# Kernel tuning notes

Measured on AMD Instinct MI355X. Metric: run time of the kernel, lower is better.

Reference implementation:

```python
import jax, jax.numpy as jnp
import numpy as np

B = 128
INPUT_SIZE = 1024
VALUE_CAP = 32768      # value_capacity (memory_size of value SDM)
VALUE_SPARSITY = 32
ASSOC_CAP = 4096       # associative_capacity; projected_size = ASSOC_CAP * 1
ASSOC_SPARSITY = 32
PROJ_DIM = ASSOC_CAP   # associative_projection_scale_factor = 1


def _row_normalize(x):
    return x / jnp.linalg.norm(x, axis=1, keepdims=True)


def setup_inputs() -> dict:
    key = jax.random.key(0)
    k1, k2, k3, k4, k5 = jax.random.split(key, 5)
    keys = jax.random.normal(k1, (B, INPUT_SIZE), dtype=jnp.float32)
    # value_memory.proj: row-normalized random projection [VALUE_CAP, INPUT_SIZE]
    value_proj = _row_normalize(jax.random.normal(k2, (VALUE_CAP, INPUT_SIZE), dtype=jnp.float32))
    # clique_encoder: randn / sqrt(projected_size) [VALUE_CAP, PROJ_DIM]
    clique_encoder = jax.random.normal(k3, (VALUE_CAP, PROJ_DIM), dtype=jnp.float32) / np.sqrt(PROJ_DIM)
    # associative_memory.proj: row-normalized [ASSOC_CAP, PROJ_DIM]
    assoc_proj = _row_normalize(jax.random.normal(k4, (ASSOC_CAP, PROJ_DIM), dtype=jnp.float32))
    # associative_memory.mem_value [ASSOC_CAP, VALUE_CAP] (zeros in a fresh
    # module; randomized here so retrieval output is non-trivial)
    assoc_mem_value = jax.random.normal(k5, (ASSOC_CAP, VALUE_CAP), dtype=jnp.float32) * 0.01
    return {
        "keys": keys,
        "value_proj": value_proj,
        "clique_encoder": clique_encoder,
        "assoc_proj": assoc_proj,
        "assoc_mem_value": assoc_mem_value,
    }


def reference(keys, value_proj, clique_encoder, assoc_proj, assoc_mem_value):
    # AssociativeSparseDistributedMemory.get_cliques(keys)
    # 1) value_memory.encode: dense matmul + topk addressing
    scores = keys @ value_proj.T                          # [B, VALUE_CAP]
    _, clique_idx = jax.lax.top_k(scores, VALUE_SPARSITY)  # [B, K]
    # 2) _dense_projection: gather K rows of clique_encoder, sum, scale, l2-normalize
    p = clique_encoder[clique_idx].sum(axis=1)            # [B, PROJ_DIM]
    p = p / np.sqrt(VALUE_SPARSITY)
    norm = jnp.linalg.norm(p, axis=-1, keepdims=True)
    p = p / jnp.maximum(norm, 1e-12)                      # F.normalize semantics
    # 3) associative_memory.get_value: encode + gather-sum retrieval
    scores2 = p @ assoc_proj.T                            # [B, ASSOC_CAP]
    _, assoc_idx = jax.lax.top_k(scores2, ASSOC_SPARSITY)  # [B, K2]
    cliques = assoc_mem_value[assoc_idx].sum(axis=1)      # [B, VALUE_CAP]
    return cliques
```

## Files before the change

kernel.cpp:

```cpp
#include <hip/hip_runtime.h>
#include <math.h>

#define TOPK 32
#define NVAL 32768
#define D 4096

typedef __attribute__((ext_vector_type(8))) short bf16x8;
typedef __attribute__((ext_vector_type(4))) float f32x4;

__device__ inline short f2bf(float x) {
    union { float f; unsigned u; } v; v.f = x;
    unsigned r = v.u + 0x7fffu + ((v.u >> 16) & 1u);
    return (short)(r >> 16);
}

__global__ __launch_bounds__(256) void cvt_bf16_kernel(
    const float* __restrict__ in, short* __restrict__ out, int n4)
{
    int i = blockIdx.x * 256 + threadIdx.x;
    if (i < n4) {
        float4 v = ((const float4*)in)[i];
        short4 o = {f2bf(v.x), f2bf(v.y), f2bf(v.z), f2bf(v.w)};
        ((short4*)out)[i] = o;
    }
}

__global__ __launch_bounds__(256) void gemm_bf16_kernel(
    const short* __restrict__ Abf, const float* __restrict__ B,
    float* __restrict__ C, int K, int N, int klen)
{
    const int t = threadIdx.x;
    const int lane = t & 63;
    const int w = t >> 6;
    const int ntile = blockIdx.x * 64 + w * 16;
    const int k0 = blockIdx.y * klen;
    float* Cb = C + (size_t)blockIdx.y * 128 * N;

    const int kfrag = (lane >> 4) * 8;
    const float* bp = B + (size_t)(ntile + (lane & 15)) * K + kfrag;
    const short* ap = Abf + (size_t)(lane & 15) * K + kfrag;

    f32x4 acc[8];
    #pragma unroll
    for (int j = 0; j < 8; ++j) acc[j] = (f32x4){0.f, 0.f, 0.f, 0.f};

    float4 x0 = *(const float4*)(bp + k0);
    float4 x1 = *(const float4*)(bp + k0 + 4);
    float4 y0 = *(const float4*)(bp + k0 + 32);
    float4 y1 = *(const float4*)(bp + k0 + 36);
    for (int ks = k0; ks < k0 + klen; ks += 32) {
        bf16x8 af;
        af[0] = f2bf(x0.x); af[1] = f2bf(x0.y); af[2] = f2bf(x0.z); af[3] = f2bf(x0.w);
        af[4] = f2bf(x1.x); af[5] = f2bf(x1.y); af[6] = f2bf(x1.z); af[7] = f2bf(x1.w);
        x0 = y0; x1 = y1;
        if (ks + 64 < k0 + klen) {
            y0 = *(const float4*)(bp + ks + 64);
            y1 = *(const float4*)(bp + ks + 68);
        }
        #pragma unroll
        for (int j = 0; j < 8; ++j) {
            bf16x8 kf = *(const bf16x8*)(ap + (size_t)16 * K * j + ks);
            acc[j] = __builtin_amdgcn_mfma_f32_16x16x32_bf16(af, kf, acc[j], 0, 0, 0);
        }
    }
    const int crow0 = ntile + (lane >> 4) * 4;
    const int ccol = lane & 15;
    #pragma unroll
    for (int j = 0; j < 8; ++j) {
        float4 o = {acc[j][0], acc[j][1], acc[j][2], acc[j][3]};
        *(float4*)(Cb + (size_t)(16 * j + ccol) * N + crow0) = o;
    }
}

__global__ __launch_bounds__(256) void reduceS_kernel(
    const float* __restrict__ part, float* __restrict__ out, int elems4, int S)
{
    int i = blockIdx.x * blockDim.x + threadIdx.x;
    if (i < elems4) {
        float4 s = {0.f, 0.f, 0.f, 0.f};
        for (int r = 0; r < S; ++r) {
            float4 v = *(const float4*)(part + (size_t)r * elems4 * 4 + (size_t)i * 4);
            s.x += v.x; s.y += v.y; s.z += v.z; s.w += v.w;
        }
        *(float4*)(out + (size_t)i * 4) = s;
    }
}

#define FNT 512
__global__ __launch_bounds__(FNT) void filter64_kernel(
    const float* __restrict__ scores, int n, int* __restrict__ cand_out)
{
    __shared__ unsigned long long lkey[8 * FNT];
    __shared__ unsigned long long wkey[FNT / 64];
    const int t = threadIdx.x;
    const float* row = scores + (size_t)blockIdx.x * n;

    unsigned long long kl[8];
    #pragma unroll
    for (int i = 0; i < 8; ++i) kl[i] = 0ull;

    const int nvec = n >> 2;
    for (int base = t; base < nvec; base += FNT) {
        float4 x4 = *(const float4*)(row + base * 4);
        float xs[4] = {x4.x, x4.y, x4.z, x4.w};
        #pragma unroll
        for (int q = 0; q < 4; ++q) {
            unsigned fb = __float_as_uint(xs[q]);
            unsigned s = (fb & 0x80000000u) ? ~fb : (fb | 0x80000000u);
            unsigned idx = (unsigned)(base * 4 + q);
            unsigned long long key = ((unsigned long long)s << 32) | (unsigned long long)(~idx);
            if (key > kl[7]) {
                unsigned long long c = key;
                #pragma unroll
                for (int i = 0; i < 8; ++i) {
                    unsigned long long old = kl[i];
                    bool gt = c > old;
                    kl[i] = gt ? c : old;
                    c = gt ? old : c;
                }
            }
        }
    }
    #pragma unroll
    for (int i = 0; i < 8; ++i) lkey[i * FNT + t] = kl[i];
    __syncthreads();

    int h = 0;
    int* out = cand_out + blockIdx.x * 64;
    for (int sel = 0; sel < 64; ++sel) {
        unsigned long long cnd = (h < 8) ? lkey[h * FNT + t] : 0ull;
        unsigned long long b = cnd;
        #pragma unroll
        for (int s2 = 1; s2 < 64; s2 <<= 1) {
            unsigned long long o = __shfl_xor(b, s2);
            if (o > b) b = o;
        }
        if ((t & 63) == 0) wkey[t >> 6] = b;
        __syncthreads();
        unsigned long long g = wkey[0];
        #pragma unroll
        for (int ww = 1; ww < FNT / 64; ++ww) {
            unsigned long long o = wkey[ww];
            if (o > g) g = o;
        }
        if (t == 0) out[sel] = (int)(~(unsigned)g);
        if (cnd == g) h++;
        __syncthreads();
    }
}

__global__ __launch_bounds__(256) void rescore_part_kernel(
    const float* __restrict__ Arows, const float* __restrict__ Brows,
    const int* __restrict__ cand, int K, unsigned long long* __restrict__ keybuf)
{
    __shared__ float arow[4096];
    const int t = threadIdx.x;
    const int b = blockIdx.x;
    const int s = blockIdx.y;
    for (int i = t; i < (K >> 2); i += 256)
        ((float4*)arow)[i] = ((const float4*)(Arows + (size_t)b * K))[i];
    __syncthreads();
    const int w = t >> 6, lane = t & 63;
    for (int c = s * 32 + w; c < s * 32 + 32; c += 4) {
        int r = cand[b * 64 + c];
        const float4* bp = (const float4*)(Brows + (size_t)r * K);
        float sum = 0.f;
        for (int q = lane; q < (K >> 2); q += 64) {
            float4 bv = bp[q];
            float4 av = ((float4*)arow)[q];
            sum = fmaf(av.x, bv.x, fmaf(av.y, bv.y, fmaf(av.z, bv.z, fmaf(av.w, bv.w, sum))));
        }
        #pragma unroll
        for (int sh = 1; sh < 64; sh <<= 1) sum += __shfl_xor(sum, sh);
        if (lane == 0) {
            unsigned fb = __float_as_uint(sum);
            unsigned ss = (fb & 0x80000000u) ? ~fb : (fb | 0x80000000u);
            keybuf[b * 64 + c] = ((unsigned long long)ss << 32) | (unsigned long long)(~(unsigned)r);
        }
    }
}

__global__ __launch_bounds__(64) void top32_keys_kernel(
    const unsigned long long* __restrict__ keybuf, int* __restrict__ idx_out)
{
    const int b = blockIdx.x, t = threadIdx.x;
    unsigned long long key = keybuf[b * 64 + t];
    int* out = idx_out + b * TOPK;
    for (int sel = 0; sel < TOPK; ++sel) {
        unsigned long long g = key;
        #pragma unroll
        for (int sh = 1; sh < 64; sh <<= 1) {
            unsigned long long o = __shfl_xor(g, sh);
            if (o > g) g = o;
        }
        if (t == 0) out[sel] = (int)(~(unsigned)g);
        if (key == g) key = 0ull;
    }
}

__global__ __launch_bounds__(256) void gather_sum_kernel(
    const float* __restrict__ enc, const int* __restrict__ idx,
    float* __restrict__ p_raw, float* __restrict__ ssp)
{
    __shared__ int rows[TOPK];
    __shared__ float red[256];
    const int t = threadIdx.x;
    const int half = blockIdx.x;
    const int b = blockIdx.y;
    if (t < TOPK) rows[t] = idx[b * TOPK + t];
    __syncthreads();
    const int base = half * 2048 + t * 8;
    float4 a0 = {}, a1 = {};
    #pragma unroll 4
    for (int r = 0; r < TOPK; ++r) {
        const float* src = enc + (size_t)rows[r] * D + base;
        float4 v0 = *(const float4*)(src);
        float4 v1 = *(const float4*)(src + 4);
        a0.x += v0.x; a0.y += v0.y; a0.z += v0.z; a0.w += v0.w;
        a1.x += v1.x; a1.y += v1.y; a1.z += v1.z; a1.w += v1.w;
    }
    const float sc = 0.17677669529663687f;
    a0.x *= sc; a0.y *= sc; a0.z *= sc; a0.w *= sc;
    a1.x *= sc; a1.y *= sc; a1.z *= sc; a1.w *= sc;
    float ss = a0.x*a0.x + a0.y*a0.y + a0.z*a0.z + a0.w*a0.w
             + a1.x*a1.x + a1.y*a1.y + a1.z*a1.z + a1.w*a1.w;
    red[t] = ss;
    __syncthreads();
    for (int s = 128; s > 0; s >>= 1) {
        if (t < s) red[t] += red[t + s];
        __syncthreads();
    }
    if (t == 0) ssp[b * 2 + half] = red[0];
    float* dst = p_raw + (size_t)b * D + base;
    *(float4*)dst = a0;
    *(float4*)(dst + 4) = a1;
}

__global__ __launch_bounds__(256) void normalize_kernel(
    const float* __restrict__ p_raw, const float* __restrict__ ssp,
    float* __restrict__ p, short* __restrict__ p_bf)
{
    const int b = blockIdx.x, t = threadIdx.x;
    const float rinv = 1.0f / fmaxf(sqrtf(ssp[b * 2] + ssp[b * 2 + 1]), 1e-12f);
    for (int i = t; i < (D >> 2); i += 256) {
        float4 v = ((const float4*)(p_raw + (size_t)b * D))[i];
        float4 o = {v.x * rinv, v.y * rinv, v.z * rinv, v.w * rinv};
        ((float4*)(p + (size_t)b * D))[i] = o;
        short4 ob = {f2bf(o.x), f2bf(o.y), f2bf(o.z), f2bf(o.w)};
        ((short4*)(p_bf + (size_t)b * D))[i] = ob;
    }
}

__global__ __launch_bounds__(256) void gather_out_kernel(
    const float* __restrict__ mem, const int* __restrict__ idx, float* __restrict__ out)
{
    extern __shared__ float throttle[];
    __shared__ int rows[TOPK];
    const int t = threadIdx.x;
    const int b = blockIdx.x;
    const int chunk = blockIdx.y;
    if (t < TOPK) rows[t] = idx[b * TOPK + t];
    __syncthreads();
    const int off = chunk * 2048 + t * 8;
    float4 a0 = {}, a1 = {};
    #pragma unroll 4
    for (int r = 0; r < TOPK; ++r) {
        const float* src = mem + (size_t)rows[r] * NVAL + off;
        float4 v0 = *(const float4*)(src);
        float4 v1 = *(const float4*)(src + 4);
        a0.x += v0.x; a0.y += v0.y; a0.z += v0.z; a0.w += v0.w;
        a1.x += v1.x; a1.y += v1.y; a1.z += v1.z; a1.w += v1.w;
    }
    if (rows[0] < 0) { throttle[t] = a0.x; out[0] = throttle[t + 1]; }
    float* dst = out + (size_t)b * NVAL + off;
    *(float4*)dst = a0;
    *(float4*)(dst + 4) = a1;
}

extern "C" void kernel_launch(void* const* d_in, const int* in_sizes, int n_in,
                              void* d_out, int out_size, void* d_ws, size_t ws_size,
                              hipStream_t stream) {
    const float* keys            = (const float*)d_in[0];
    const float* value_proj      = (const float*)d_in[1];
    const float* clique_encoder  = (const float*)d_in[2];
    const float* assoc_proj      = (const float*)d_in[3];
    const float* assoc_mem_value = (const float*)d_in[4];
    float* out = (float*)d_out;

    char* ws = (char*)d_ws;
    short* keysbf = (short*)(ws);
    float* s1a    = (float*)(ws + 262144);
    float* p_raw  = (float*)(ws + 17039360);
    float* p      = (float*)(ws + 19136512);
    short* p_bf   = (short*)(ws + 21233664);
    float* part2  = (float*)(ws + 22282240);
    float* s2a    = (float*)(ws + 30670848);
    int*   cand1  = (int*)  (ws + 32768000);
    int*   cand2  = (int*)  (ws + 32800768);
    int*   idx1   = (int*)  (ws + 32833536);
    int*   idx2   = (int*)  (ws + 32849920);
    unsigned long long* keyb1 = (unsigned long long*)(ws + 32866304);
    unsigned long long* keyb2 = (unsigned long long*)(ws + 32931840);
    float* ssp    = (float*)(ws + 32997376);

    cvt_bf16_kernel<<<128, 256, 0, stream>>>(keys, keysbf, 32768);
    gemm_bf16_kernel<<<dim3(512, 1), 256, 0, stream>>>(keysbf, value_proj, s1a, 1024, NVAL, 1024);
    filter64_kernel<<<128, FNT, 0, stream>>>(s1a, NVAL, cand1);
    rescore_part_kernel<<<dim3(128, 2), 256, 0, stream>>>(keys, value_proj, cand1, 1024, keyb1);
    top32_keys_kernel<<<128, 64, 0, stream>>>(keyb1, idx1);
    gather_sum_kernel<<<dim3(2, 128), 256, 0, stream>>>(clique_encoder, idx1, p_raw, ssp);
    normalize_kernel<<<128, 256, 0, stream>>>(p_raw, ssp, p, p_bf);
    gemm_bf16_kernel<<<dim3(64, 4), 256, 0, stream>>>(p_bf, assoc_proj, part2, 4096, D, 1024);
    reduceS_kernel<<<512, 256, 0, stream>>>(part2, s2a, 131072, 4);
    filter64_kernel<<<128, FNT, 0, stream>>>(s2a, D, cand2);
    rescore_part_kernel<<<dim3(128, 2), 256, 0, stream>>>(p, assoc_proj, cand2, 4096, keyb2);
    top32_keys_kernel<<<128, 64, 0, stream>>>(keyb2, idx2);
    gather_out_kernel<<<dim3(128, 16), 256, 40960, stream>>>(assoc_mem_value, idx2, out);
}
```

Before: 445.2 us.

## Use split-bf16 GEMM for second stage and skip rescore when top-32 gap is clear

The second scoring GEMM now uses a hi/lo bf16 split of the normalized projection (three MFMAs per tile) so its scores are near-fp32 accurate. A new select2 kernel fuses the split-K reduction into the top-64 filter, writes the top-32 indices directly, and flags rows whose 32nd/33rd gap is below a threshold. Only flagged rows run the exact fp32 rescore and top-32 pass. The first GEMM gains a deeper prefetch and the first rescore grid doubles in the y dimension. The price is three times the MFMA work plus an extra lo buffer, and correctness now depends on the 1e-5 gap threshold being safe.

```diff
diff --git a/kernel.cpp b/kernel.cpp
--- a/kernel.cpp
+++ b/kernel.cpp
@@ -12,6 +12,10 @@
     union { float f; unsigned u; } v; v.f = x;
     unsigned r = v.u + 0x7fffu + ((v.u >> 16) & 1u);
     return (short)(r >> 16);
+}
+__device__ inline float bf2f(short h) {
+    union { unsigned u; float f; } v; v.u = ((unsigned)(unsigned short)h) << 16;
+    return v.f;
 }
 
 __global__ __launch_bounds__(256) void cvt_bf16_kernel(
@@ -27,7 +31,54 @@
 
 __global__ __launch_bounds__(256) void gemm_bf16_kernel(
     const short* __restrict__ Abf, const float* __restrict__ B,
-    float* __restrict__ C, int K, int N, int klen)
+    float* __restrict__ C, int K, int N)
+{
+    const int t = threadIdx.x;
+    const int lane = t & 63;
+    const int w = t >> 6;
+    const int ntile = blockIdx.x * 64 + w * 16;
+
+    const int kfrag = (lane >> 4) * 8;
+    const float* bp = B + (size_t)(ntile + (lane & 15)) * K + kfrag;
+    const short* ap = Abf + (size_t)(lane & 15) * K + kfrag;
+
+    f32x4 acc[8];
+    #pragma unroll
+    for (int j = 0; j < 8; ++j) acc[j] = (f32x4){0.f, 0.f, 0.f, 0.f};
+
+    float4 x0 = *(const float4*)(bp);
+    float4 x1 = *(const float4*)(bp + 4);
+    float4 y0 = *(const float4*)(bp + 32);
+    float4 y1 = *(const float4*)(bp + 36);
+    float4 z0 = *(const float4*)(bp + 64);
+    float4 z1 = *(const float4*)(bp + 68);
+    for (int ks = 0; ks < K; ks += 32) {
+        bf16x8 af;
+        af[0] = f2bf(x0.x); af[1] = f2bf(x0.y); af[2] = f2bf(x0.z); af[3] = f2bf(x0.w);
+        af[4] = f2bf(x1.x); af[5] = f2bf(x1.y); af[6] = f2bf(x1.z); af[7] = f2bf(x1.w);
+        x0 = y0; x1 = y1; y0 = z0; y1 = z1;
+        if (ks + 96 < K) {
+            z0 = *(const float4*)(bp + ks + 96);
+            z1 = *(const float4*)(bp + ks + 100);
+        }
+        #pragma unroll
+        for (int j = 0; j < 8; ++j) {
+            bf16x8 kf = *(const bf16x8*)(ap + (size_t)16 * K * j + ks);
+            acc[j] = __builtin_amdgcn_mfma_f32_16x16x32_bf16(af, kf, acc[j], 0, 0, 0);
+        }
+    }
+    const int crow0 = ntile + (lane >> 4) * 4;
+    const int ccol = lane & 15;
+    #pragma unroll
+    for (int j = 0; j < 8; ++j) {
+        float4 o = {acc[j][0], acc[j][1], acc[j][2], acc[j][3]};
+        *(float4*)(C + (size_t)(16 * j + ccol) * N + crow0) = o;
+    }
+}
+
+__global__ __launch_bounds__(256) void gemm_split_kernel(
+    const short* __restrict__ Ahi, const short* __restrict__ Alo,
+    const float* __restrict__ B, float* __restrict__ C, int K, int N, int klen)
 {
     const int t = threadIdx.x;
     const int lane = t & 63;
@@ -38,7 +89,8 @@
 
     const int kfrag = (lane >> 4) * 8;
     const float* bp = B + (size_t)(ntile + (lane & 15)) * K + kfrag;
-    const short* ap = Abf + (size_t)(lane & 15) * K + kfrag;
+    const short* aph = Ahi + (size_t)(lane & 15) * K + kfrag;
+    const short* apl = Alo + (size_t)(lane & 15) * K + kfrag;
 
     f32x4 acc[8];
     #pragma unroll
@@ -49,18 +101,26 @@
     float4 y0 = *(const float4*)(bp + k0 + 32);
     float4 y1 = *(const float4*)(bp + k0 + 36);
     for (int ks = k0; ks < k0 + klen; ks += 32) {
-        bf16x8 af;
-        af[0] = f2bf(x0.x); af[1] = f2bf(x0.y); af[2] = f2bf(x0.z); af[3] = f2bf(x0.w);
-        af[4] = f2bf(x1.x); af[5] = f2bf(x1.y); af[6] = f2bf(x1.z); af[7] = f2bf(x1.w);
+        float xs[8] = {x0.x, x0.y, x0.z, x0.w, x1.x, x1.y, x1.z, x1.w};
         x0 = y0; x1 = y1;
         if (ks + 64 < k0 + klen) {
             y0 = *(const float4*)(bp + ks + 64);
             y1 = *(const float4*)(bp + ks + 68);
         }
+        bf16x8 bh, bl;
+        #pragma unroll
+        for (int q = 0; q < 8; ++q) {
+            short h = f2bf(xs[q]);
+            bh[q] = h;
+            bl[q] = f2bf(xs[q] - bf2f(h));
+        }
         #pragma unroll
         for (int j = 0; j < 8; ++j) {
-            bf16x8 kf = *(const bf16x8*)(ap + (size_t)16 * K * j + ks);
-            acc[j] = __builtin_amdgcn_mfma_f32_16x16x32_bf16(af, kf, acc[j], 0, 0, 0);
+            bf16x8 kh = *(const bf16x8*)(aph + (size_t)16 * K * j + ks);
+            bf16x8 kl = *(const bf16x8*)(apl + (size_t)16 * K * j + ks);
+            acc[j] = __builtin_amdgcn_mfma_f32_16x16x32_bf16(bh, kh, acc[j], 0, 0, 0);
+            acc[j] = __builtin_amdgcn_mfma_f32_16x16x32_bf16(bl, kh, acc[j], 0, 0, 0);
+            acc[j] = __builtin_amdgcn_mfma_f32_16x16x32_bf16(bh, kl, acc[j], 0, 0, 0);
         }
     }
     const int crow0 = ntile + (lane >> 4) * 4;
@@ -69,20 +129,6 @@
     for (int j = 0; j < 8; ++j) {
         float4 o = {acc[j][0], acc[j][1], acc[j][2], acc[j][3]};
         *(float4*)(Cb + (size_t)(16 * j + ccol) * N + crow0) = o;
-    }
-}
-
-__global__ __launch_bounds__(256) void reduceS_kernel(
-    const float* __restrict__ part, float* __restrict__ out, int elems4, int S)
-{
-    int i = blockIdx.x * blockDim.x + threadIdx.x;
-    if (i < elems4) {
-        float4 s = {0.f, 0.f, 0.f, 0.f};
-        for (int r = 0; r < S; ++r) {
-            float4 v = *(const float4*)(part + (size_t)r * elems4 * 4 + (size_t)i * 4);
-            s.x += v.x; s.y += v.y; s.z += v.z; s.w += v.w;
-        }
-        *(float4*)(out + (size_t)i * 4) = s;
     }
 }
 
@@ -149,19 +195,98 @@
     }
 }
 
+__global__ __launch_bounds__(FNT) void select2_kernel(
+    const float* __restrict__ part, int n, int* __restrict__ idx_out,
+    int* __restrict__ cand_out, int* __restrict__ flags)
+{
+    __shared__ unsigned long long lkey[8 * FNT];
+    __shared__ unsigned long long wkey[FNT / 64];
+    const int t = threadIdx.x;
+    const int b = blockIdx.x;
+
+    unsigned long long kl[8];
+    #pragma unroll
+    for (int i = 0; i < 8; ++i) kl[i] = 0ull;
+
+    const int nvec = n >> 2;
+    for (int base = t; base < nvec; base += FNT) {
+        float4 s0 = *(const float4*)(part + ((size_t)0 * 128 + b) * n + base * 4);
+        float4 s1 = *(const float4*)(part + ((size_t)1 * 128 + b) * n + base * 4);
+        float4 s2 = *(const float4*)(part + ((size_t)2 * 128 + b) * n + base * 4);
+        float4 s3 = *(const float4*)(part + ((size_t)3 * 128 + b) * n + base * 4);
+        float xs[4] = {s0.x + s1.x + s2.x + s3.x, s0.y + s1.y + s2.y + s3.y,
+                       s0.z + s1.z + s2.z + s3.z, s0.w + s1.w + s2.w + s3.w};
+        #pragma unroll
+        for (int q = 0; q < 4; ++q) {
+            unsigned fb = __float_as_uint(xs[q]);
+            unsigned s = (fb & 0x80000000u) ? ~fb : (fb | 0x80000000u);
+            unsigned idx = (unsigned)(base * 4 + q);
+            unsigned long long key = ((unsigned long long)s << 32) | (unsigned long long)(~idx);
+            if (key > kl[7]) {
+                unsigned long long c = key;
+                #pragma unroll
+                for (int i = 0; i < 8; ++i) {
+                    unsigned long long old = kl[i];
+                    bool gt = c > old;
+                    kl[i] = gt ? c : old;
+                    c = gt ? old : c;
+                }
+            }
+        }
+    }
+    #pragma unroll
+    for (int i = 0; i < 8; ++i) lkey[i * FNT + t] = kl[i];
+    __syncthreads();
+
+    int h = 0;
+    float v31 = 0.f, v32 = 0.f;
+    for (int sel = 0; sel < 64; ++sel) {
+        unsigned long long cnd = (h < 8) ? lkey[h * FNT + t] : 0ull;
+        unsigned long long bk = cnd;
+        #pragma unroll
+        for (int s2 = 1; s2 < 64; s2 <<= 1) {
+            unsigned long long o = __shfl_xor(bk, s2);
+            if (o > bk) bk = o;
+        }
+        if ((t & 63) == 0) wkey[t >> 6] = bk;
+        __syncthreads();
+        unsigned long long g = wkey[0];
+        #pragma unroll
+        for (int ww = 1; ww < FNT / 64; ++ww) {
+            unsigned long long o = wkey[ww];
+            if (o > g) g = o;
+        }
+        if (t == 0) {
+            cand_out[b * 64 + sel] = (int)(~(unsigned)g);
+            if (sel < TOPK) idx_out[b * TOPK + sel] = (int)(~(unsigned)g);
+            unsigned hi = (unsigned)(g >> 32);
+            float val = (hi & 0x80000000u) ? __uint_as_float(hi ^ 0x80000000u)
+                                           : __uint_as_float(~hi);
+            if (sel == 31) v31 = val;
+            if (sel == 32) v32 = val;
+        }
+        if (cnd == g) h++;
+        __syncthreads();
+    }
+    if (t == 0) flags[b] = (v31 - v32 < 1e-5f) ? 1 : 0;
+}
+
 __global__ __launch_bounds__(256) void rescore_part_kernel(
     const float* __restrict__ Arows, const float* __restrict__ Brows,
-    const int* __restrict__ cand, int K, unsigned long long* __restrict__ keybuf)
+    const int* __restrict__ cand, int K, unsigned long long* __restrict__ keybuf,
+    const int* __restrict__ flags)
 {
     __shared__ float arow[4096];
     const int t = threadIdx.x;
     const int b = blockIdx.x;
+    if (flags && !flags[b]) return;
     const int s = blockIdx.y;
+    const int cper = 64 / gridDim.y;
     for (int i = t; i < (K >> 2); i += 256)
         ((float4*)arow)[i] = ((const float4*)(Arows + (size_t)b * K))[i];
     __syncthreads();
     const int w = t >> 6, lane = t & 63;
-    for (int c = s * 32 + w; c < s * 32 + 32; c += 4) {
+    for (int c = s * cper + w; c < s * cper + cper; c += 4) {
         int r = cand[b * 64 + c];
         const float4* bp = (const float4*)(Brows + (size_t)r * K);
         float sum = 0.f;
@@ -181,9 +306,11 @@
 }
 
 __global__ __launch_bounds__(64) void top32_keys_kernel(
-    const unsigned long long* __restrict__ keybuf, int* __restrict__ idx_out)
+    const unsigned long long* __restrict__ keybuf, int* __restrict__ idx_out,
+    const int* __restrict__ flags)
 {
     const int b = blockIdx.x, t = threadIdx.x;
+    if (flags && !flags[b]) return;
     unsigned long long key = keybuf[b * 64 + t];
     int* out = idx_out + b * TOPK;
     for (int sel = 0; sel < TOPK; ++sel) {
@@ -238,7 +365,7 @@
 
 __global__ __launch_bounds__(256) void normalize_kernel(
     const float* __restrict__ p_raw, const float* __restrict__ ssp,
-    float* __restrict__ p, short* __restrict__ p_bf)
+    float* __restrict__ p, short* __restrict__ p_hi, short* __restrict__ p_lo)
 {
     const int b = blockIdx.x, t = threadIdx.x;
     const float rinv = 1.0f / fmaxf(sqrtf(ssp[b * 2] + ssp[b * 2 + 1]), 1e-12f);
@@ -246,8 +373,11 @@
         float4 v = ((const float4*)(p_raw + (size_t)b * D))[i];
         float4 o = {v.x * rinv, v.y * rinv, v.z * rinv, v.w * rinv};
         ((float4*)(p + (size_t)b * D))[i] = o;
-        short4 ob = {f2bf(o.x), f2bf(o.y), f2bf(o.z), f2bf(o.w)};
-        ((short4*)(p_bf + (size_t)b * D))[i] = ob;
+        short4 oh = {f2bf(o.x), f2bf(o.y), f2bf(o.z), f2bf(o.w)};
+        short4 ol = {f2bf(o.x - bf2f(oh.x)), f2bf(o.y - bf2f(oh.y)),
+                     f2bf(o.z - bf2f(oh.z)), f2bf(o.w - bf2f(oh.w))};
+        ((short4*)(p_hi + (size_t)b * D))[i] = oh;
+        ((short4*)(p_lo + (size_t)b * D))[i] = ol;
     }
 }
 
@@ -292,28 +422,28 @@
     float* s1a    = (float*)(ws + 262144);
     float* p_raw  = (float*)(ws + 17039360);
     float* p      = (float*)(ws + 19136512);
-    short* p_bf   = (short*)(ws + 21233664);
-    float* part2  = (float*)(ws + 22282240);
-    float* s2a    = (float*)(ws + 30670848);
-    int*   cand1  = (int*)  (ws + 32768000);
-    int*   cand2  = (int*)  (ws + 32800768);
-    int*   idx1   = (int*)  (ws + 32833536);
-    int*   idx2   = (int*)  (ws + 32849920);
-    unsigned long long* keyb1 = (unsigned long long*)(ws + 32866304);
-    unsigned long long* keyb2 = (unsigned long long*)(ws + 32931840);
-    float* ssp    = (float*)(ws + 32997376);
+    short* p_hi   = (short*)(ws + 21233664);
+    short* p_lo   = (short*)(ws + 22282240);
+    float* part2  = (float*)(ws + 23330816);
+    int*   cand1  = (int*)  (ws + 31719424);
+    int*   cand2  = (int*)  (ws + 31752192);
+    int*   idx1   = (int*)  (ws + 31784960);
+    int*   idx2   = (int*)  (ws + 31801344);
+    unsigned long long* keyb1 = (unsigned long long*)(ws + 31817728);
+    unsigned long long* keyb2 = (unsigned long long*)(ws + 31883264);
+    float* ssp    = (float*)(ws + 31948800);
+    int*   flags  = (int*)  (ws + 31949824);
 
     cvt_bf16_kernel<<<128, 256, 0, stream>>>(keys, keysbf, 32768);
-    gemm_bf16_kernel<<<dim3(512, 1), 256, 0, stream>>>(keysbf, value_proj, s1a, 1024, NVAL, 1024);
+    gemm_bf16_kernel<<<dim3(512), 256, 0, stream>>>(keysbf, value_proj, s1a, 1024, NVAL);
     filter64_kernel<<<128, FNT, 0, stream>>>(s1a, NVAL, cand1);
-    rescore_part_kernel<<<dim3(128, 2), 256, 0, stream>>>(keys, value_proj, cand1, 1024, keyb1);
-    top32_keys_kernel<<<128, 64, 0, stream>>>(keyb1, idx1);
+    rescore_part_kernel<<<dim3(128, 4), 256, 0, stream>>>(keys, value_proj, cand1, 1024, keyb1, nullptr);
+    top32_keys_kernel<<<128, 64, 0, stream>>>(keyb1, idx1, nullptr);
     gather_sum_kernel<<<dim3(2, 128), 256, 0, stream>>>(clique_encoder, idx1, p_raw, ssp);
-    normalize_kernel<<<128, 256, 0, stream>>>(p_raw, ssp, p, p_bf);
-    gemm_bf16_kernel<<<dim3(64, 4), 256, 0, stream>>>(p_bf, assoc_proj, part2, 4096, D, 1024);
-    reduceS_kernel<<<512, 256, 0, stream>>>(part2, s2a, 131072, 4);
-    filter64_kernel<<<128, FNT, 0, stream>>>(s2a, D, cand2);
-    rescore_part_kernel<<<dim3(128, 2), 256, 0, stream>>>(p, assoc_proj, cand2, 4096, keyb2);
-    top32_keys_kernel<<<128, 64, 0, stream>>>(keyb2, idx2);
+    normalize_kernel<<<128, 256, 0, stream>>>(p_raw, ssp, p, p_hi, p_lo);
+    gemm_split_kernel<<<dim3(64, 4), 256, 0, stream>>>(p_hi, p_lo, assoc_proj, part2, D, D, 1024);
+    select2_kernel<<<128, FNT, 0, stream>>>(part2, D, idx2, cand2, flags);
+    rescore_part_kernel<<<dim3(128, 2), 256, 0, stream>>>(p, assoc_proj, cand2, 4096, keyb2, flags);
+    top32_keys_kernel<<<128, 64, 0, stream>>>(keyb2, idx2, flags);
     gather_out_kernel<<<dim3(128, 16), 256, 40960, stream>>>(assoc_mem_value, idx2, out);
 }
```

New measurement: 480.2 us. +7.9%, slower.

## Use split-bf16 GEMMs and skip fp32 rescoring when top-k margin is clear

Applied to the files above, without the earlier changes.

Both score GEMMs now split the operands into hi and lo bf16 parts and issue three MFMAs per step, giving near-fp32 accuracy. The selection kernel writes the top-32 indices directly and sets a per-row flag only when the gap between the 32nd and 33rd scores is below an epsilon. Rescoring and the final top-32 run only for flagged rows, which saves the fp32 candidate rescoring on most rows. In exchange the GEMMs do triple the MFMA work plus extra lo-operand loads, and the second GEMM is split further along K (8 slices) with a larger partial-sum reduction.

```diff
diff --git a/kernel.cpp b/kernel.cpp
--- a/kernel.cpp
+++ b/kernel.cpp
@@ -13,21 +13,28 @@
     unsigned r = v.u + 0x7fffu + ((v.u >> 16) & 1u);
     return (short)(r >> 16);
 }
-
-__global__ __launch_bounds__(256) void cvt_bf16_kernel(
-    const float* __restrict__ in, short* __restrict__ out, int n4)
+__device__ inline float bf2f(short h) {
+    union { unsigned u; float f; } v; v.u = ((unsigned)(unsigned short)h) << 16;
+    return v.f;
+}
+
+__global__ __launch_bounds__(256) void cvt_split_kernel(
+    const float* __restrict__ in, short* __restrict__ hi, short* __restrict__ lo, int n4)
 {
     int i = blockIdx.x * 256 + threadIdx.x;
     if (i < n4) {
         float4 v = ((const float4*)in)[i];
-        short4 o = {f2bf(v.x), f2bf(v.y), f2bf(v.z), f2bf(v.w)};
-        ((short4*)out)[i] = o;
-    }
-}
-
-__global__ __launch_bounds__(256) void gemm_bf16_kernel(
-    const short* __restrict__ Abf, const float* __restrict__ B,
-    float* __restrict__ C, int K, int N, int klen)
+        short4 h = {f2bf(v.x), f2bf(v.y), f2bf(v.z), f2bf(v.w)};
+        short4 l = {f2bf(v.x - bf2f(h.x)), f2bf(v.y - bf2f(h.y)),
+                    f2bf(v.z - bf2f(h.z)), f2bf(v.w - bf2f(h.w))};
+        ((short4*)hi)[i] = h;
+        ((short4*)lo)[i] = l;
+    }
+}
+
+__global__ __launch_bounds__(256) void gemm_split_kernel(
+    const short* __restrict__ Ahi, const short* __restrict__ Alo,
+    const float* __restrict__ B, float* __restrict__ C, int K, int N, int klen)
 {
     const int t = threadIdx.x;
     const int lane = t & 63;
@@ -38,7 +45,8 @@
 
     const int kfrag = (lane >> 4) * 8;
     const float* bp = B + (size_t)(ntile + (lane & 15)) * K + kfrag;
-    const short* ap = Abf + (size_t)(lane & 15) * K + kfrag;
+    const short* aph = Ahi + (size_t)(lane & 15) * K + kfrag;
+    const short* apl = Alo + (size_t)(lane & 15) * K + kfrag;
 
     f32x4 acc[8];
     #pragma unroll
@@ -49,18 +57,26 @@
     float4 y0 = *(const float4*)(bp + k0 + 32);
     float4 y1 = *(const float4*)(bp + k0 + 36);
     for (int ks = k0; ks < k0 + klen; ks += 32) {
-        bf16x8 af;
-        af[0] = f2bf(x0.x); af[1] = f2bf(x0.y); af[2] = f2bf(x0.z); af[3] = f2bf(x0.w);
-        af[4] = f2bf(x1.x); af[5] = f2bf(x1.y); af[6] = f2bf(x1.z); af[7] = f2bf(x1.w);
+        float xs[8] = {x0.x, x0.y, x0.z, x0.w, x1.x, x1.y, x1.z, x1.w};
         x0 = y0; x1 = y1;
         if (ks + 64 < k0 + klen) {
             y0 = *(const float4*)(bp + ks + 64);
             y1 = *(const float4*)(bp + ks + 68);
         }
+        bf16x8 bh, bl;
+        #pragma unroll
+        for (int q = 0; q < 8; ++q) {
+            short h = f2bf(xs[q]);
+            bh[q] = h;
+            bl[q] = f2bf(xs[q] - bf2f(h));
+        }
         #pragma unroll
         for (int j = 0; j < 8; ++j) {
-            bf16x8 kf = *(const bf16x8*)(ap + (size_t)16 * K * j + ks);
-            acc[j] = __builtin_amdgcn_mfma_f32_16x16x32_bf16(af, kf, acc[j], 0, 0, 0);
+            bf16x8 kh = *(const bf16x8*)(aph + (size_t)16 * K * j + ks);
+            bf16x8 kl = *(const bf16x8*)(apl + (size_t)16 * K * j + ks);
+            acc[j] = __builtin_amdgcn_mfma_f32_16x16x32_bf16(bh, kh, acc[j], 0, 0, 0);
+            acc[j] = __builtin_amdgcn_mfma_f32_16x16x32_bf16(bl, kh, acc[j], 0, 0, 0);
+            acc[j] = __builtin_amdgcn_mfma_f32_16x16x32_bf16(bh, kl, acc[j], 0, 0, 0);
         }
     }
     const int crow0 = ntile + (lane >> 4) * 4;
@@ -87,13 +103,15 @@
 }
 
 #define FNT 512
-__global__ __launch_bounds__(FNT) void filter64_kernel(
-    const float* __restrict__ scores, int n, int* __restrict__ cand_out)
+__global__ __launch_bounds__(FNT) void select_kernel(
+    const float* __restrict__ scores, int n, int* __restrict__ idx_out,
+    int* __restrict__ cand_out, int* __restrict__ flags, float eps)
 {
     __shared__ unsigned long long lkey[8 * FNT];
     __shared__ unsigned long long wkey[FNT / 64];
     const int t = threadIdx.x;
-    const float* row = scores + (size_t)blockIdx.x * n;
+    const int b = blockIdx.x;
+    const float* row = scores + (size_t)b * n;
 
     unsigned long long kl[8];
     #pragma unroll
@@ -126,16 +144,16 @@
     __syncthreads();
 
     int h = 0;
-    int* out = cand_out + blockIdx.x * 64;
+    float v31 = 0.f, v32 = 0.f;
     for (int sel = 0; sel < 64; ++sel) {
         unsigned long long cnd = (h < 8) ? lkey[h * FNT + t] : 0ull;
-        unsigned long long b = cnd;
+        unsigned long long bk = cnd;
         #pragma unroll
         for (int s2 = 1; s2 < 64; s2 <<= 1) {
-            unsigned long long o = __shfl_xor(b, s2);
-            if (o > b) b = o;
-        }
-        if ((t & 63) == 0) wkey[t >> 6] = b;
+            unsigned long long o = __shfl_xor(bk, s2);
+            if (o > bk) bk = o;
+        }
+        if ((t & 63) == 0) wkey[t >> 6] = bk;
         __syncthreads();
         unsigned long long g = wkey[0];
         #pragma unroll
@@ -143,25 +161,37 @@
             unsigned long long o = wkey[ww];
             if (o > g) g = o;
         }
-        if (t == 0) out[sel] = (int)(~(unsigned)g);
+        if (t == 0) {
+            cand_out[b * 64 + sel] = (int)(~(unsigned)g);
+            if (sel < TOPK) idx_out[b * TOPK + sel] = (int)(~(unsigned)g);
+            unsigned hi = (unsigned)(g >> 32);
+            float val = (hi & 0x80000000u) ? __uint_as_float(hi ^ 0x80000000u)
+                                           : __uint_as_float(~hi);
+            if (sel == 31) v31 = val;
+            if (sel == 32) v32 = val;
+        }
         if (cnd == g) h++;
         __syncthreads();
     }
+    if (t == 0) flags[b] = (v31 - v32 < eps) ? 1 : 0;
 }
 
 __global__ __launch_bounds__(256) void rescore_part_kernel(
     const float* __restrict__ Arows, const float* __restrict__ Brows,
-    const int* __restrict__ cand, int K, unsigned long long* __restrict__ keybuf)
+    const int* __restrict__ cand, int K, unsigned long long* __restrict__ keybuf,
+    const int* __restrict__ flags)
 {
     __shared__ float arow[4096];
     const int t = threadIdx.x;
     const int b = blockIdx.x;
+    if (!flags[b]) return;
     const int s = blockIdx.y;
+    const int cper = 64 / gridDim.y;
     for (int i = t; i < (K >> 2); i += 256)
         ((float4*)arow)[i] = ((const float4*)(Arows + (size_t)b * K))[i];
     __syncthreads();
     const int w = t >> 6, lane = t & 63;
-    for (int c = s * 32 + w; c < s * 32 + 32; c += 4) {
+    for (int c = s * cper + w; c < s * cper + cper; c += 4) {
         int r = cand[b * 64 + c];
         const float4* bp = (const float4*)(Brows + (size_t)r * K);
         float sum = 0.f;
@@ -181,9 +211,11 @@
 }
 
 __global__ __launch_bounds__(64) void top32_keys_kernel(
-    const unsigned long long* __restrict__ keybuf, int* __restrict__ idx_out)
+    const unsigned long long* __restrict__ keybuf, int* __restrict__ idx_out,
+    const int* __restrict__ flags)
 {
     const int b = blockIdx.x, t = threadIdx.x;
+    if (!flags[b]) return;
     unsigned long long key = keybuf[b * 64 + t];
     int* out = idx_out + b * TOPK;
     for (int sel = 0; sel < TOPK; ++sel) {
@@ -238,7 +270,7 @@
 
 __global__ __launch_bounds__(256) void normalize_kernel(
     const float* __restrict__ p_raw, const float* __restrict__ ssp,
-    float* __restrict__ p, short* __restrict__ p_bf)
+    float* __restrict__ p, short* __restrict__ p_hi, short* __restrict__ p_lo)
 {
     const int b = blockIdx.x, t = threadIdx.x;
     const float rinv = 1.0f / fmaxf(sqrtf(ssp[b * 2] + ssp[b * 2 + 1]), 1e-12f);
@@ -246,8 +278,11 @@
         float4 v = ((const float4*)(p_raw + (size_t)b * D))[i];
         float4 o = {v.x * rinv, v.y * rinv, v.z * rinv, v.w * rinv};
         ((float4*)(p + (size_t)b * D))[i] = o;
-        short4 ob = {f2bf(o.x), f2bf(o.y), f2bf(o.z), f2bf(o.w)};
-        ((short4*)(p_bf + (size_t)b * D))[i] = ob;
+        short4 oh = {f2bf(o.x), f2bf(o.y), f2bf(o.z), f2bf(o.w)};
+        short4 ol = {f2bf(o.x - bf2f(oh.x)), f2bf(o.y - bf2f(oh.y)),
+                     f2bf(o.z - bf2f(oh.z)), f2bf(o.w - bf2f(oh.w))};
+        ((short4*)(p_hi + (size_t)b * D))[i] = oh;
+        ((short4*)(p_lo + (size_t)b * D))[i] = ol;
     }
 }
 
@@ -288,32 +323,36 @@
     float* out = (float*)d_out;
 
     char* ws = (char*)d_ws;
-    short* keysbf = (short*)(ws);
-    float* s1a    = (float*)(ws + 262144);
-    float* p_raw  = (float*)(ws + 17039360);
-    float* p      = (float*)(ws + 19136512);
-    short* p_bf   = (short*)(ws + 21233664);
-    float* part2  = (float*)(ws + 22282240);
-    float* s2a    = (float*)(ws + 30670848);
-    int*   cand1  = (int*)  (ws + 32768000);
-    int*   cand2  = (int*)  (ws + 32800768);
-    int*   idx1   = (int*)  (ws + 32833536);
-    int*   idx2   = (int*)  (ws + 32849920);
-    unsigned long long* keyb1 = (unsigned long long*)(ws + 32866304);
-    unsigned long long* keyb2 = (unsigned long long*)(ws + 32931840);
-    float* ssp    = (float*)(ws + 32997376);
-
-    cvt_bf16_kernel<<<128, 256, 0, stream>>>(keys, keysbf, 32768);
-    gemm_bf16_kernel<<<dim3(512, 1), 256, 0, stream>>>(keysbf, value_proj, s1a, 1024, NVAL, 1024);
-    filter64_kernel<<<128, FNT, 0, stream>>>(s1a, NVAL, cand1);
-    rescore_part_kernel<<<dim3(128, 2), 256, 0, stream>>>(keys, value_proj, cand1, 1024, keyb1);
-    top32_keys_kernel<<<128, 64, 0, stream>>>(keyb1, idx1);
+    short* keys_hi = (short*)(ws);
+    short* keys_lo = (short*)(ws + 262144);
+    float* s1a     = (float*)(ws + 524288);
+    float* p_raw   = (float*)(ws + 17301504);
+    float* p       = (float*)(ws + 19398656);
+    short* p_hi    = (short*)(ws + 21495808);
+    short* p_lo    = (short*)(ws + 22544384);
+    float* part2   = (float*)(ws + 23592960);
+    float* s2a     = (float*)(ws + 40370176);
+    int*   cand1   = (int*)  (ws + 42467328);
+    int*   cand2   = (int*)  (ws + 42500096);
+    int*   idx1    = (int*)  (ws + 42532864);
+    int*   idx2    = (int*)  (ws + 42549248);
+    unsigned long long* keyb1 = (unsigned long long*)(ws + 42565632);
+    unsigned long long* keyb2 = (unsigned long long*)(ws + 42631168);
+    float* ssp     = (float*)(ws + 42696704);
+    int*   flags1  = (int*)  (ws + 42697728);
+    int*   flags2  = (int*)  (ws + 42698240);
+
+    cvt_split_kernel<<<128, 256, 0, stream>>>(keys, keys_hi, keys_lo, 32768);
+    gemm_split_kernel<<<dim3(512, 1), 256, 0, stream>>>(keys_hi, keys_lo, value_proj, s1a, 1024, NVAL, 1024);
+    select_kernel<<<128, FNT, 0, stream>>>(s1a, NVAL, idx1, cand1, flags1, 2e-4f);
+    rescore_part_kernel<<<dim3(128, 4), 256, 0, stream>>>(keys, value_proj, cand1, 1024, keyb1, flags1);
+    top32_keys_kernel<<<128, 64, 0, stream>>>(keyb1, idx1, flags1);
     gather_sum_kernel<<<dim3(2, 128), 256, 0, stream>>>(clique_encoder, idx1, p_raw, ssp);
-    normalize_kernel<<<128, 256, 0, stream>>>(p_raw, ssp, p, p_bf);
-    gemm_bf16_kernel<<<dim3(64, 4), 256, 0, stream>>>(p_bf, assoc_proj, part2, 4096, D, 1024);
-    reduceS_kernel<<<512, 256, 0, stream>>>(part2, s2a, 131072, 4);
-    filter64_kernel<<<128, FNT, 0, stream>>>(s2a, D, cand2);
-    rescore_part_kernel<<<dim3(128, 2), 256, 0, stream>>>(p, assoc_proj, cand2, 4096, keyb2);
-    top32_keys_kernel<<<128, 64, 0, stream>>>(keyb2, idx2);
+    normalize_kernel<<<128, 256, 0, stream>>>(p_raw, ssp, p, p_hi, p_lo);
+    gemm_split_kernel<<<dim3(64, 8), 256, 0, stream>>>(p_hi, p_lo, assoc_proj, part2, 4096, D, 512);
+    reduceS_kernel<<<512, 256, 0, stream>>>(part2, s2a, 131072, 8);
+    select_kernel<<<128, FNT, 0, stream>>>(s2a, D, idx2, cand2, flags2, 1e-5f);
+    rescore_part_kernel<<<dim3(128, 4), 256, 0, stream>>>(p, assoc_proj, cand2, 4096, keyb2, flags2);
+    top32_keys_kernel<<<128, 64, 0, stream>>>(keyb2, idx2, flags2);
     gather_out_kernel<<<dim3(128, 16), 256, 40960, stream>>>(assoc_mem_value, idx2, out);
 }
```

New measurement: 486.8 us. 9.3% more time.
